# Kernel optimization log

Hardware: AMD Instinct MI355X
Metric: run time of the kernel (lower is better)

The kernel has to match this reference:

```python
import jax, jax.numpy as jnp
import numpy as np

B, N, D, H, CD = 2, 2048, 1024, 16, 3
HD = D // H


def setup_inputs() -> dict:
    key = jax.random.key(0)
    ks = jax.random.split(key, 6)
    x = jax.random.normal(ks[0], (B, N, D), dtype=jnp.float32)
    coords = jax.random.normal(ks[1], (B, N, CD), dtype=jnp.float32)
    attn_bias = jax.random.normal(ks[2], (N, N), dtype=jnp.float32) * 0.1
    Wqkv = jax.random.normal(ks[3], (D, 3 * D), dtype=jnp.float32) * (1.0 / np.sqrt(D))
    bqkv = jnp.zeros((3 * D,), dtype=jnp.float32)
    rel_weight = jax.random.normal(ks[4], (H, CD), dtype=jnp.float32) * 0.02
    return {"x": x, "coords": coords, "attn_bias": attn_bias, "Wqkv": Wqkv,
            "bqkv": bqkv, "rel_weight": rel_weight}


def reference(x, coords, attn_bias, Wqkv, bqkv, rel_weight):
    b, n, d = x.shape
    h, hd = H, HD
    qkv = x @ Wqkv + bqkv                       # (B,N,3D)
    q, k, v = jnp.split(qkv, 3, axis=-1)
    # reshape_for_mha: (B,N,D) -> (B,H,N,hd)
    def heads(t):
        return t.reshape(b, n, h, hd).transpose(0, 2, 1, 3)
    qh, kh, vh = heads(q), heads(k), heads(v)
    # coord_proj[b,h,n] = coords[b,n,:] @ rel_weight[h,:]
    coord_proj = jnp.einsum('bnc,hc->bhn', coords.astype(jnp.float32), rel_weight)
    # flex_attention: scale by 1/sqrt(head_dim) BEFORE score_mod
    scores = jnp.einsum('bhqd,bhkd->bhqk', qh, kh) / np.sqrt(hd)
    scores = scores + coord_proj[:, :, :, None] - coord_proj[:, :, None, :]
    scores = scores + attn_bias[None, None, :, :]   # '2d' additive mask bias
    attn = jax.nn.softmax(scores, axis=-1)
    yh = jnp.einsum('bhqk,bhkd->bhqd', attn, vh)    # (B,H,N,hd)
    return yh.transpose(0, 2, 1, 3).reshape(b, n, d)
```

## Files before the change

kernel.cpp:

```cpp
#include <hip/hip_runtime.h>
#include <hip/hip_bf16.h>
#include <math.h>

typedef __hip_bfloat16 bf16;
typedef __bf16  bf16x8 __attribute__((ext_vector_type(8)));
typedef float   f32x4  __attribute__((ext_vector_type(4)));

#define BB 2
#define NN 2048
#define DD 1024
#define HH 16
#define HD 64
#define LOG2E   1.44269504f
#define SCALE_Q 0.18033688f

__device__ __forceinline__ void glds16(const bf16* g, bf16* l) {
    __builtin_amdgcn_global_load_lds((const __attribute__((address_space(1))) void*)g,
                                     (__attribute__((address_space(3))) void*)l, 16, 0, 0);
}
__device__ __forceinline__ unsigned short bfu(float x) {
    bf16 b = __float2bfloat16(x);
    return __builtin_bit_cast(unsigned short, b);
}

__global__ __launch_bounds__(256) void prep(const float* __restrict__ x,
                                            const float* __restrict__ bias,
                                            const float* __restrict__ W,
                                            const float* __restrict__ coords,
                                            const float* __restrict__ relw,
                                            bf16* __restrict__ xb,
                                            float* __restrict__ pbf,
                                            bf16* __restrict__ Wt,
                                            bf16* __restrict__ cpn) {
    __shared__ bf16 tsm[64][65];
    const int bid = blockIdx.x, tid = threadIdx.x;
    if (bid < 2048) {
        size_t i = ((size_t)bid * 256 + tid) * 8;
        float4 a = *(const float4*)(x + i);
        float4 b = *(const float4*)(x + i + 4);
        bf16 t[8];
        t[0] = __float2bfloat16(a.x); t[1] = __float2bfloat16(a.y);
        t[2] = __float2bfloat16(a.z); t[3] = __float2bfloat16(a.w);
        t[4] = __float2bfloat16(b.x); t[5] = __float2bfloat16(b.y);
        t[6] = __float2bfloat16(b.z); t[7] = __float2bfloat16(b.w);
        *(int4*)(xb + i) = *(int4*)t;
    } else if (bid < 3072) {
        int t    = (bid - 2048) * 256 + tid;
        int lane = t & 63;
        int wave = (t >> 6) & 7;
        int kt   = (t >> 9) & 31;
        int Qb   = t >> 14;
        int quad = lane >> 4, l15 = lane & 15;
        float v[16];
#pragma unroll
        for (int j = 0; j < 16; ++j) {
            int g = j >> 2, r = j & 3;
            int q = Qb * 128 + wave * 16 + quad * 4 + r;
            int k = kt * 64 + g * 16 + l15;
            v[j] = LOG2E * bias[(size_t)q * NN + k];
        }
        int4* dst = (int4*)(pbf + (size_t)t * 16);
#pragma unroll
        for (int i = 0; i < 4; ++i) dst[i] = ((int4*)v)[i];
    } else if (bid < 3840) {
        int idx = bid - 3072;
        int n0 = (idx % 48) * 64;
        int k0 = (idx / 48) * 64;
        int tx = tid & 63, tg = tid >> 6;
#pragma unroll
        for (int i = 0; i < 16; ++i) {
            int r = tg + i * 4;
            tsm[r][tx] = __float2bfloat16(W[(size_t)(k0 + r) * 3072 + n0 + tx]);
        }
        __syncthreads();
#pragma unroll
        for (int i = 0; i < 16; ++i) {
            int r = tg + i * 4;
            Wt[(size_t)(n0 + r) * 1024 + k0 + tx] = tsm[tx][r];
        }
    } else {
        int idx = (bid - 3840) * 256 + tid;
        int n  = idx & (NN - 1);
        int bh = idx >> 11;
        int h  = bh & (HH - 1);
        int b  = bh >> 4;
        float acc = 0.f;
#pragma unroll
        for (int c = 0; c < 3; ++c)
            acc += coords[(size_t)(b * NN + n) * 3 + c] * relw[h * 3 + c];
        cpn[idx] = __float2bfloat16(-LOG2E * acc);
    }
}

__global__ __launch_bounds__(256) void qkv_gemm(const bf16* __restrict__ X,
                                                const bf16* __restrict__ W,
                                                const float* __restrict__ bq,
                                                bf16* __restrict__ qo,
                                                bf16* __restrict__ ko,
                                                bf16* __restrict__ vt) {
    __shared__ __align__(16) bf16 As[128 * 32];
    __shared__ __align__(16) bf16 Bs[128 * 32];
    const int tid  = threadIdx.x;
    const int n0   = blockIdx.x * 128;
    const int m0   = blockIdx.y * 128;
    const int wave = tid >> 6, lane = tid & 63, l15 = lane & 15, quad = lane >> 4;
    const int wm   = wave >> 1, wn = wave & 1;

    f32x4 acc[4][4];
    const f32x4 z4 = {0.f, 0.f, 0.f, 0.f};
#pragma unroll
    for (int i = 0; i < 4; ++i)
#pragma unroll
        for (int j = 0; j < 4; ++j) acc[i][j] = z4;

    for (int kt = 0; kt < 1024; kt += 32) {
        __syncthreads();
#pragma unroll
        for (int j = 0; j < 2; ++j) {
            int s   = (wave * 2 + j) * 64 + lane;
            int row = s >> 2;
            int c   = (s & 3) ^ ((row >> 1) & 3);
            glds16(X + (size_t)(m0 + row) * 1024 + kt + c * 8, As + (wave * 2 + j) * 512);
            glds16(W + (size_t)(n0 + row) * 1024 + kt + c * 8, Bs + (wave * 2 + j) * 512);
        }
        __syncthreads();

        bf16x8 a[4], b[4];
#pragma unroll
        for (int mt = 0; mt < 4; ++mt) {
            int ra = wm * 64 + mt * 16 + l15;
            a[mt] = *(const bf16x8*)&As[ra * 32 + ((quad ^ ((ra >> 1) & 3)) * 8)];
        }
#pragma unroll
        for (int nt = 0; nt < 4; ++nt) {
            int rb = wn * 64 + nt * 16 + l15;
            b[nt] = *(const bf16x8*)&Bs[rb * 32 + ((quad ^ ((rb >> 1) & 3)) * 8)];
        }
#pragma unroll
        for (int mt = 0; mt < 4; ++mt)
#pragma unroll
            for (int nt = 0; nt < 4; ++nt)
                acc[mt][nt] = __builtin_amdgcn_mfma_f32_16x16x32_bf16(a[mt], b[nt], acc[mt][nt], 0, 0, 0);
    }

#pragma unroll
    for (int nt = 0; nt < 4; ++nt) {
        int c    = n0 + wn * 64 + nt * 16 + l15;
        int tsel = c >> 10;
        int rem  = c & 1023;
        int h    = rem >> 6, d = rem & 63;
        float bias = bq[c];
        float qs   = (tsel == 0) ? SCALE_Q : 1.0f;
#pragma unroll
        for (int mt = 0; mt < 4; ++mt)
#pragma unroll
            for (int r = 0; r < 4; ++r) {
                int m = m0 + wm * 64 + mt * 16 + quad * 4 + r;
                int b = m >> 11, n = m & (NN - 1);
                bf16 val = __float2bfloat16((acc[mt][nt][r] + bias) * qs);
                if (tsel == 2)
                    vt[((size_t)(b * HH + h) * HD + d) * NN + n] = val;
                else
                    ((tsel == 1) ? ko : qo)[((size_t)(b * HH + h) * NN + n) * HD + d] = val;
            }
    }
}

__global__ __launch_bounds__(512, 4) void attn(const bf16* __restrict__ Q,
                                               const bf16* __restrict__ K,
                                               const bf16* __restrict__ Vt_g,
                                               const bf16* __restrict__ cpn_g,
                                               const float* __restrict__ pbf,
                                               float* __restrict__ out) {
    __shared__ __align__(16) bf16 Ks[2][64 * 64];
    __shared__ __align__(16) bf16 Vs[2][64 * 64];
    __shared__ __align__(16) unsigned PsW[8][16 * 36];
    __shared__ __align__(16) bf16 cpl[NN];
    const int tid  = threadIdx.x;
    const int Qb   = blockIdx.x;
    const int bh   = blockIdx.y;
    const int b    = bh >> 4, h = bh & 15;
    const int q0   = Qb * 128;
    const int wave = tid >> 6, lane = tid & 63, l15 = lane & 15, quad = lane >> 4;
    const size_t base = (size_t)bh * NN * HD;

    if (wave < 4)
        glds16(cpn_g + bh * NN + (wave * 64 + lane) * 8, cpl + wave * 512);

    const int qrow = q0 + wave * 16 + l15;
    bf16x8 qf0 = *(const bf16x8*)&Q[base + (size_t)qrow * HD + quad * 8];
    bf16x8 qf1 = *(const bf16x8*)&Q[base + (size_t)qrow * HD + 32 + quad * 8];

    const int ps   = wave * 64 + lane;
    const int prow = ps >> 3;
    const int pcol = (ps & 7) ^ (prow & 7);

    glds16(K    + base + (size_t)prow * HD + pcol * 8, Ks[0] + wave * 512);
    glds16(Vt_g + base + (size_t)prow * NN + pcol * 8, Vs[0] + wave * 512);

    const float* bptr = pbf + ((((size_t)Qb * 32) * 8 + wave) * 64 + lane) * 16;
    float4 bvA[4], bvB[4];
#pragma unroll
    for (int i = 0; i < 4; ++i) bvA[i] = ((const float4*)bptr)[i];

    const f32x4 z4 = {0.f, 0.f, 0.f, 0.f};
    f32x4 l4 = z4;
    f32x4 o[4];
#pragma unroll
    for (int t = 0; t < 4; ++t) o[t] = z4;

#define ATTN_TILE(T, CUR, BVC, BVN)                                               \
    {                                                                             \
        __syncthreads();     \
        if ((T) < 31) {                   \
            int kk1 = ((T) + 1) * 64;                                             \
            glds16(K    + base + (size_t)(kk1 + prow) * HD + pcol * 8,            \
                   Ks[(CUR) ^ 1] + wave * 512);                                   \
            glds16(Vt_g + base + (size_t)prow * NN + kk1 + pcol * 8,              \
                   Vs[(CUR) ^ 1] + wave * 512);                                   \
            const float* bp = bptr + (size_t)((T) + 1) * 8192;                    \
            BVN[0] = ((const float4*)bp)[0];                                      \
            BVN[1] = ((const float4*)bp)[1];                                      \
            BVN[2] = ((const float4*)bp)[2];                                      \
            BVN[3] = ((const float4*)bp)[3];                                      \
        }                                                                         \
            \
        f32x4 p4[4];                                                              \
        _Pragma("unroll")                                                         \
        for (int g = 0; g < 4; ++g) {                                             \
            float mgv = __bfloat162float(cpl[(T) * 64 + g * 16 + l15]);           \
            f32x4 mg4 = {mgv, mgv, mgv, mgv};                                     \
            f32x4 c0  = __builtin_bit_cast(f32x4, BVC[g]) + mg4;                  \
            int krow = g * 16 + l15, sw = krow & 7;                               \
            bf16x8 k0 = *(const bf16x8*)&Ks[(CUR)][krow * 64 + ((quad ^ sw) * 8)];         \
            bf16x8 k1 = *(const bf16x8*)&Ks[(CUR)][krow * 64 + (((4 + quad) ^ sw) * 8)];   \
            f32x4 s4 = __builtin_amdgcn_mfma_f32_16x16x32_bf16(qf0, k0, c0, 0, 0, 0);      \
            s4 = __builtin_amdgcn_mfma_f32_16x16x32_bf16(qf1, k1, s4, 0, 0, 0);   \
            f32x4 e;                                                              \
            e[0] = __builtin_amdgcn_exp2f(s4[0]);                                 \
            e[1] = __builtin_amdgcn_exp2f(s4[1]);                                 \
            e[2] = __builtin_amdgcn_exp2f(s4[2]);                                 \
            e[3] = __builtin_amdgcn_exp2f(s4[3]);                                 \
            p4[g] = e;                                                            \
            l4 = l4 + e;                                                          \
        }                                                                         \
                  \
        _Pragma("unroll")                                                         \
        for (int g2 = 0; g2 < 2; ++g2)                                            \
            _Pragma("unroll")                                                     \
            for (int r = 0; r < 4; ++r) {                                         \
                unsigned pk = (unsigned)bfu(p4[g2][r]) |                          \
                              ((unsigned)bfu(p4[g2 + 2][r]) << 16);               \
                PsW[wave][(quad * 4 + r) * 36 + g2 * 16 + l15] = pk;              \
            }                                                                     \
        asm volatile("s_waitcnt lgkmcnt(0)" ::: "memory");                        \
        const int4* pr = (const int4*)&PsW[wave][l15 * 36 + quad * 8];            \
        int4 da = pr[0], db = pr[1];                                              \
        union { unsigned u[4]; bf16x8 v; } u0, u1;                                \
        u0.u[0] = __builtin_amdgcn_perm(da.y, da.x, 0x05040100u);                 \
        u0.u[1] = __builtin_amdgcn_perm(da.w, da.z, 0x05040100u);                 \
        u0.u[2] = __builtin_amdgcn_perm(db.y, db.x, 0x05040100u);                 \
        u0.u[3] = __builtin_amdgcn_perm(db.w, db.z, 0x05040100u);                 \
        u1.u[0] = __builtin_amdgcn_perm(da.y, da.x, 0x07060302u);                 \
        u1.u[1] = __builtin_amdgcn_perm(da.w, da.z, 0x07060302u);                 \
        u1.u[2] = __builtin_amdgcn_perm(db.y, db.x, 0x07060302u);                 \
        u1.u[3] = __builtin_amdgcn_perm(db.w, db.z, 0x07060302u);                 \
                                              \
        __builtin_amdgcn_s_setprio(1);                                            \
        _Pragma("unroll")                                                         \
        for (int tt = 0; tt < 4; ++tt) {                                          \
            int drow = tt * 16 + l15, sw2 = drow & 7;                             \
            bf16x8 v0 = *(const bf16x8*)&Vs[(CUR)][drow * 64 + ((quad ^ sw2) * 8)];        \
            bf16x8 v1 = *(const bf16x8*)&Vs[(CUR)][drow * 64 + (((4 + quad) ^ sw2) * 8)];  \
            o[tt] = __builtin_amdgcn_mfma_f32_16x16x32_bf16(u0.v, v0, o[tt], 0, 0, 0);     \
            o[tt] = __builtin_amdgcn_mfma_f32_16x16x32_bf16(u1.v, v1, o[tt], 0, 0, 0);     \
        }                                                                         \
        __builtin_amdgcn_s_setprio(0);                                            \
    }

    for (int t = 0; t < 32; t += 2) {
        ATTN_TILE(t,     0, bvA, bvB)
        ATTN_TILE(t + 1, 1, bvB, bvA)
    }
#undef ATTN_TILE

    float l_loc[4] = {l4[0], l4[1], l4[2], l4[3]};
#pragma unroll
    for (int r = 0; r < 4; ++r) {
#pragma unroll
        for (int d = 1; d < 16; d <<= 1)
            l_loc[r] += __shfl_xor(l_loc[r], d, 64);
        float inv = 1.0f / l_loc[r];
        int qq = q0 + wave * 16 + quad * 4 + r;
#pragma unroll
        for (int tt = 0; tt < 4; ++tt)
            out[((size_t)(b * NN + qq)) * DD + h * HD + tt * 16 + l15] =
                o[tt][r] * inv;
    }
}

extern "C" void kernel_launch(void* const* d_in, const int* in_sizes, int n_in,
                              void* d_out, int out_size, void* d_ws, size_t ws_size,
                              hipStream_t stream) {
    const float* x      = (const float*)d_in[0];
    const float* coords = (const float*)d_in[1];
    const float* abias  = (const float*)d_in[2];
    const float* Wqkv   = (const float*)d_in[3];
    const float* bqkv   = (const float*)d_in[4];
    const float* relw   = (const float*)d_in[5];
    float* out = (float*)d_out;

    char* ws = (char*)d_ws;
    bf16*  xb  = (bf16*)(ws);
    bf16*  qw  = (bf16*)(ws + 8388608);
    bf16*  kw  = (bf16*)(ws + 16777216);
    bf16*  vt  = (bf16*)(ws + 25165824);
    bf16*  Wt  = (bf16*)(ws + 33554432);
    float* pbf = (float*)(ws + 39845888);
    bf16*  cpb = (bf16*)(ws + 56623104);

    prep    <<<dim3(4096),   256, 0, stream>>>(x, abias, Wqkv, coords, relw,
                                               xb, pbf, Wt, cpb);
    qkv_gemm<<<dim3(24, 32), 256, 0, stream>>>(xb, Wt, bqkv, qw, kw, vt);
    attn    <<<dim3(16, 32), 512, 0, stream>>>(qw, kw, vt, cpb, pbf, out);
}
```

Baseline: 203.5 us.

## Split attention key tiles across wave pairs with 64-query blocks and LDS reduction

Each attention block now covers 64 queries instead of 128, which doubles the grid. The two waves of a pair each handle half of every 64-key tile and merge their partial outputs and row sums through shared memory at the end. The bias prep kernel rewrites the pre-swizzled bias layout to match, and launch bounds are raised to allow more resident blocks. The aim is more parallelism and occupancy, at the cost of loading K/V once per 64 queries instead of once per 128, plus an extra reduction with two barriers.

```diff
diff --git a/kernel.cpp b/kernel.cpp
--- a/kernel.cpp
+++ b/kernel.cpp
@@ -45,21 +45,21 @@
         t[6] = __float2bfloat16(b.z); t[7] = __float2bfloat16(b.w);
         *(int4*)(xb + i) = *(int4*)t;
     } else if (bid < 3072) {
-        int t    = (bid - 2048) * 256 + tid;
-        int lane = t & 63;
-        int wave = (t >> 6) & 7;
-        int kt   = (t >> 9) & 31;
-        int Qb   = t >> 14;
-        int quad = lane >> 4, l15 = lane & 15;
+        int f0 = ((bid - 2048) * 256 + tid) * 16;
         float v[16];
 #pragma unroll
-        for (int j = 0; j < 16; ++j) {
-            int g = j >> 2, r = j & 3;
-            int q = Qb * 128 + wave * 16 + quad * 4 + r;
-            int k = kt * 64 + g * 16 + l15;
-            v[j] = LOG2E * bias[(size_t)q * NN + k];
-        }
-        int4* dst = (int4*)(pbf + (size_t)t * 16);
+        for (int u = 0; u < 16; ++u) {
+            int f    = f0 + u;
+            int j    = f & 7;
+            int lane = (f >> 3) & 63;
+            int wave = (f >> 9) & 7;
+            int t    = (f >> 12) & 31;
+            int Qb   = f >> 17;
+            int q = Qb * 64 + ((wave >> 1) << 4) + ((lane >> 4) << 2) + (j & 3);
+            int k = t * 64 + ((wave & 1) << 5) + ((j >> 2) << 4) + (lane & 15);
+            v[u] = LOG2E * bias[(size_t)q * NN + k];
+        }
+        int4* dst = (int4*)(pbf + (size_t)f0);
 #pragma unroll
         for (int i = 0; i < 4; ++i) dst[i] = ((int4*)v)[i];
     } else if (bid < 3840) {
@@ -166,7 +166,7 @@
     }
 }
 
-__global__ __launch_bounds__(512, 4) void attn(const bf16* __restrict__ Q,
+__global__ __launch_bounds__(512, 6) void attn(const bf16* __restrict__ Q,
                                                const bf16* __restrict__ K,
                                                const bf16* __restrict__ Vt_g,
                                                const bf16* __restrict__ cpn_g,
@@ -174,20 +174,21 @@
                                                float* __restrict__ out) {
     __shared__ __align__(16) bf16 Ks[2][64 * 64];
     __shared__ __align__(16) bf16 Vs[2][64 * 64];
-    __shared__ __align__(16) unsigned PsW[8][16 * 36];
+    __shared__ __align__(16) unsigned PsW[8][16 * 20];
     __shared__ __align__(16) bf16 cpl[NN];
     const int tid  = threadIdx.x;
     const int Qb   = blockIdx.x;
     const int bh   = blockIdx.y;
     const int b    = bh >> 4, h = bh & 15;
-    const int q0   = Qb * 128;
+    const int q0   = Qb * 64;
     const int wave = tid >> 6, lane = tid & 63, l15 = lane & 15, quad = lane >> 4;
+    const int wq   = wave >> 1, ws = wave & 1;
     const size_t base = (size_t)bh * NN * HD;
 
     if (wave < 4)
         glds16(cpn_g + bh * NN + (wave * 64 + lane) * 8, cpl + wave * 512);
 
-    const int qrow = q0 + wave * 16 + l15;
+    const int qrow = q0 + wq * 16 + l15;
     bf16x8 qf0 = *(const bf16x8*)&Q[base + (size_t)qrow * HD + quad * 8];
     bf16x8 qf1 = *(const bf16x8*)&Q[base + (size_t)qrow * HD + 32 + quad * 8];
 
@@ -198,10 +199,10 @@
     glds16(K    + base + (size_t)prow * HD + pcol * 8, Ks[0] + wave * 512);
     glds16(Vt_g + base + (size_t)prow * NN + pcol * 8, Vs[0] + wave * 512);
 
-    const float* bptr = pbf + ((((size_t)Qb * 32) * 8 + wave) * 64 + lane) * 16;
-    float4 bvA[4], bvB[4];
-#pragma unroll
-    for (int i = 0; i < 4; ++i) bvA[i] = ((const float4*)bptr)[i];
+    const float* bptr = pbf + (((size_t)(Qb * 32) * 8 + wave) * 64 + lane) * 8;
+    float4 bvA[2], bvB[2];
+    bvA[0] = ((const float4*)bptr)[0];
+    bvA[1] = ((const float4*)bptr)[1];
 
     const f32x4 z4 = {0.f, 0.f, 0.f, 0.f};
     f32x4 l4 = z4;
@@ -218,20 +219,18 @@
                    Ks[(CUR) ^ 1] + wave * 512);                                   \
             glds16(Vt_g + base + (size_t)prow * NN + kk1 + pcol * 8,              \
                    Vs[(CUR) ^ 1] + wave * 512);                                   \
-            const float* bp = bptr + (size_t)((T) + 1) * 8192;                    \
+            const float* bp = bptr + (size_t)((T) + 1) * 4096;                    \
             BVN[0] = ((const float4*)bp)[0];                                      \
             BVN[1] = ((const float4*)bp)[1];                                      \
-            BVN[2] = ((const float4*)bp)[2];                                      \
-            BVN[3] = ((const float4*)bp)[3];                                      \
         }                                                                         \
-            \
-        f32x4 p4[4];                                                              \
+                       \
+        f32x4 p4[2];                                                              \
         _Pragma("unroll")                                                         \
-        for (int g = 0; g < 4; ++g) {                                             \
-            float mgv = __bfloat162float(cpl[(T) * 64 + g * 16 + l15]);           \
+        for (int g = 0; g < 2; ++g) {                                             \
+            float mgv = __bfloat162float(cpl[(T) * 64 + ws * 32 + g * 16 + l15]); \
             f32x4 mg4 = {mgv, mgv, mgv, mgv};                                     \
             f32x4 c0  = __builtin_bit_cast(f32x4, BVC[g]) + mg4;                  \
-            int krow = g * 16 + l15, sw = krow & 7;                               \
+            int krow = ws * 32 + g * 16 + l15, sw = krow & 7;                     \
             bf16x8 k0 = *(const bf16x8*)&Ks[(CUR)][krow * 64 + ((quad ^ sw) * 8)];         \
             bf16x8 k1 = *(const bf16x8*)&Ks[(CUR)][krow * 64 + (((4 + quad) ^ sw) * 8)];   \
             f32x4 s4 = __builtin_amdgcn_mfma_f32_16x16x32_bf16(qf0, k0, c0, 0, 0, 0);      \
@@ -244,36 +243,28 @@
             p4[g] = e;                                                            \
             l4 = l4 + e;                                                          \
         }                                                                         \
-                  \
+           \
         _Pragma("unroll")                                                         \
-        for (int g2 = 0; g2 < 2; ++g2)                                            \
-            _Pragma("unroll")                                                     \
-            for (int r = 0; r < 4; ++r) {                                         \
-                unsigned pk = (unsigned)bfu(p4[g2][r]) |                          \
-                              ((unsigned)bfu(p4[g2 + 2][r]) << 16);               \
-                PsW[wave][(quad * 4 + r) * 36 + g2 * 16 + l15] = pk;              \
-            }                                                                     \
+        for (int r = 0; r < 4; ++r) {                                             \
+            unsigned pk = (unsigned)bfu(p4[0][r]) | ((unsigned)bfu(p4[1][r]) << 16); \
+            PsW[wave][(quad * 4 + r) * 20 + l15] = pk;                            \
+        }                                                                         \
         asm volatile("s_waitcnt lgkmcnt(0)" ::: "memory");                        \
-        const int4* pr = (const int4*)&PsW[wave][l15 * 36 + quad * 8];            \
+        const int4* pr = (const int4*)&PsW[wave][l15 * 20 + (quad & 1) * 8];      \
         int4 da = pr[0], db = pr[1];                                              \
-        union { unsigned u[4]; bf16x8 v; } u0, u1;                                \
-        u0.u[0] = __builtin_amdgcn_perm(da.y, da.x, 0x05040100u);                 \
-        u0.u[1] = __builtin_amdgcn_perm(da.w, da.z, 0x05040100u);                 \
-        u0.u[2] = __builtin_amdgcn_perm(db.y, db.x, 0x05040100u);                 \
-        u0.u[3] = __builtin_amdgcn_perm(db.w, db.z, 0x05040100u);                 \
-        u1.u[0] = __builtin_amdgcn_perm(da.y, da.x, 0x07060302u);                 \
-        u1.u[1] = __builtin_amdgcn_perm(da.w, da.z, 0x07060302u);                 \
-        u1.u[2] = __builtin_amdgcn_perm(db.y, db.x, 0x07060302u);                 \
-        u1.u[3] = __builtin_amdgcn_perm(db.w, db.z, 0x07060302u);                 \
-                                              \
+        union { unsigned u[4]; bf16x8 v; } uu;                                    \
+        unsigned sel = (quad < 2) ? 0x05040100u : 0x07060302u;                    \
+        uu.u[0] = __builtin_amdgcn_perm(da.y, da.x, sel);                         \
+        uu.u[1] = __builtin_amdgcn_perm(da.w, da.z, sel);                         \
+        uu.u[2] = __builtin_amdgcn_perm(db.y, db.x, sel);                         \
+        uu.u[3] = __builtin_amdgcn_perm(db.w, db.z, sel);                         \
+                                        \
         __builtin_amdgcn_s_setprio(1);                                            \
         _Pragma("unroll")                                                         \
         for (int tt = 0; tt < 4; ++tt) {                                          \
             int drow = tt * 16 + l15, sw2 = drow & 7;                             \
-            bf16x8 v0 = *(const bf16x8*)&Vs[(CUR)][drow * 64 + ((quad ^ sw2) * 8)];        \
-            bf16x8 v1 = *(const bf16x8*)&Vs[(CUR)][drow * 64 + (((4 + quad) ^ sw2) * 8)];  \
-            o[tt] = __builtin_amdgcn_mfma_f32_16x16x32_bf16(u0.v, v0, o[tt], 0, 0, 0);     \
-            o[tt] = __builtin_amdgcn_mfma_f32_16x16x32_bf16(u1.v, v1, o[tt], 0, 0, 0);     \
+            bf16x8 vf = *(const bf16x8*)&Vs[(CUR)][drow * 64 + (((ws * 4 + quad) ^ sw2) * 8)]; \
+            o[tt] = __builtin_amdgcn_mfma_f32_16x16x32_bf16(uu.v, vf, o[tt], 0, 0, 0);     \
         }                                                                         \
         __builtin_amdgcn_s_setprio(0);                                            \
     }
@@ -286,16 +277,38 @@
 
     float l_loc[4] = {l4[0], l4[1], l4[2], l4[3]};
 #pragma unroll
-    for (int r = 0; r < 4; ++r) {
+    for (int r = 0; r < 4; ++r)
 #pragma unroll
         for (int d = 1; d < 16; d <<= 1)
             l_loc[r] += __shfl_xor(l_loc[r], d, 64);
-        float inv = 1.0f / l_loc[r];
-        int qq = q0 + wave * 16 + quad * 4 + r;
-#pragma unroll
-        for (int tt = 0; tt < 4; ++tt)
-            out[((size_t)(b * NN + qq)) * DD + h * HD + tt * 16 + l15] =
-                o[tt][r] * inv;
+
+    float* obase = (wq < 2) ? (float*)Ks : (float*)Vs;
+    const int rowl0 = (wq & 1) * 16;
+    __syncthreads();
+    if (ws == 1) {
+#pragma unroll
+        for (int r = 0; r < 4; ++r) {
+            int row = rowl0 + quad * 4 + r;
+#pragma unroll
+            for (int tt = 0; tt < 4; ++tt)
+                obase[row * 68 + tt * 16 + l15] = o[tt][r];
+            if (l15 == 0) obase[row * 68 + 64] = l_loc[r];
+        }
+    }
+    __syncthreads();
+    if (ws == 0) {
+#pragma unroll
+        for (int r = 0; r < 4; ++r) {
+            int row = rowl0 + quad * 4 + r;
+            float lt  = l_loc[r] + obase[row * 68 + 64];
+            float inv = 1.0f / lt;
+            int qq = q0 + wq * 16 + quad * 4 + r;
+#pragma unroll
+            for (int tt = 0; tt < 4; ++tt) {
+                float ov = o[tt][r] + obase[row * 68 + tt * 16 + l15];
+                out[((size_t)(b * NN + qq)) * DD + h * HD + tt * 16 + l15] = ov * inv;
+            }
+        }
     }
 }
 
@@ -322,5 +335,5 @@
     prep    <<<dim3(4096),   256, 0, stream>>>(x, abias, Wqkv, coords, relw,
                                                xb, pbf, Wt, cpb);
     qkv_gemm<<<dim3(24, 32), 256, 0, stream>>>(xb, Wt, bqkv, qw, kw, vt);
-    attn    <<<dim3(16, 32), 512, 0, stream>>>(qw, kw, vt, cpb, pbf, out);
-}
+    attn    <<<dim3(32, 32), 512, 0, stream>>>(qw, kw, vt, cpb, pbf, out);
+}
```

Result: slower. 232.8 us (+14.4%).

## Process two 16-row query tiles per wave in attention, halve block size

Applied to the files above, without the earlier changes.

Each wave now handles 32 query rows (two 16-row sub-tiles) instead of 16. The K and V fragments read from LDS are reused across both sub-tiles, and the block shrinks from 512 to 256 threads. The bias pre-layout in the prep kernel is reordered to match the new per-wave fragment mapping. This cuts LDS read traffic and synchronisation per unit of work, at the cost of more registers per thread and fewer waves per block to hide latency.

```diff
diff --git a/kernel.cpp b/kernel.cpp
--- a/kernel.cpp
+++ b/kernel.cpp
@@ -45,21 +45,22 @@
         t[6] = __float2bfloat16(b.z); t[7] = __float2bfloat16(b.w);
         *(int4*)(xb + i) = *(int4*)t;
     } else if (bid < 3072) {
-        int t    = (bid - 2048) * 256 + tid;
-        int lane = t & 63;
-        int wave = (t >> 6) & 7;
-        int kt   = (t >> 9) & 31;
-        int Qb   = t >> 14;
-        int quad = lane >> 4, l15 = lane & 15;
+        int f0 = ((bid - 2048) * 256 + tid) * 16;
         float v[16];
 #pragma unroll
-        for (int j = 0; j < 16; ++j) {
-            int g = j >> 2, r = j & 3;
-            int q = Qb * 128 + wave * 16 + quad * 4 + r;
-            int k = kt * 64 + g * 16 + l15;
-            v[j] = LOG2E * bias[(size_t)q * NN + k];
-        }
-        int4* dst = (int4*)(pbf + (size_t)t * 16);
+        for (int u = 0; u < 16; ++u) {
+            int f    = f0 + u;
+            int j    = f & 15;
+            int lane = (f >> 4) & 63;
+            int qh   = (f >> 10) & 1;
+            int w    = (f >> 11) & 3;
+            int t    = (f >> 13) & 31;
+            int Qb   = f >> 18;
+            int q = Qb * 128 + w * 32 + qh * 16 + ((lane >> 4) << 2) + (j & 3);
+            int k = t * 64 + ((j >> 2) << 4) + (lane & 15);
+            v[u] = LOG2E * bias[(size_t)q * NN + k];
+        }
+        int4* dst = (int4*)(pbf + (size_t)f0);
 #pragma unroll
         for (int i = 0; i < 4; ++i) dst[i] = ((int4*)v)[i];
     } else if (bid < 3840) {
@@ -166,7 +167,7 @@
     }
 }
 
-__global__ __launch_bounds__(512, 4) void attn(const bf16* __restrict__ Q,
+__global__ __launch_bounds__(256, 2) void attn(const bf16* __restrict__ Q,
                                                const bf16* __restrict__ K,
                                                const bf16* __restrict__ Vt_g,
                                                const bf16* __restrict__ cpn_g,
@@ -174,128 +175,195 @@
                                                float* __restrict__ out) {
     __shared__ __align__(16) bf16 Ks[2][64 * 64];
     __shared__ __align__(16) bf16 Vs[2][64 * 64];
-    __shared__ __align__(16) unsigned PsW[8][16 * 36];
+    __shared__ __align__(16) unsigned PsW[4][16 * 36];
     __shared__ __align__(16) bf16 cpl[NN];
     const int tid  = threadIdx.x;
     const int Qb   = blockIdx.x;
     const int bh   = blockIdx.y;
     const int b    = bh >> 4, h = bh & 15;
     const int q0   = Qb * 128;
-    const int wave = tid >> 6, lane = tid & 63, l15 = lane & 15, quad = lane >> 4;
+    const int w    = tid >> 6, lane = tid & 63, l15 = lane & 15, quad = lane >> 4;
     const size_t base = (size_t)bh * NN * HD;
 
-    if (wave < 4)
-        glds16(cpn_g + bh * NN + (wave * 64 + lane) * 8, cpl + wave * 512);
-
-    const int qrow = q0 + wave * 16 + l15;
-    bf16x8 qf0 = *(const bf16x8*)&Q[base + (size_t)qrow * HD + quad * 8];
-    bf16x8 qf1 = *(const bf16x8*)&Q[base + (size_t)qrow * HD + 32 + quad * 8];
-
-    const int ps   = wave * 64 + lane;
-    const int prow = ps >> 3;
-    const int pcol = (ps & 7) ^ (prow & 7);
-
-    glds16(K    + base + (size_t)prow * HD + pcol * 8, Ks[0] + wave * 512);
-    glds16(Vt_g + base + (size_t)prow * NN + pcol * 8, Vs[0] + wave * 512);
-
-    const float* bptr = pbf + ((((size_t)Qb * 32) * 8 + wave) * 64 + lane) * 16;
-    float4 bvA[4], bvB[4];
-#pragma unroll
-    for (int i = 0; i < 4; ++i) bvA[i] = ((const float4*)bptr)[i];
+    glds16(cpn_g + bh * NN + (w * 64 + lane) * 8, cpl + w * 512);
+
+    const int qr0 = q0 + w * 32 + l15;
+    bf16x8 qf00 = *(const bf16x8*)&Q[base + (size_t)qr0 * HD + quad * 8];
+    bf16x8 qf01 = *(const bf16x8*)&Q[base + (size_t)qr0 * HD + 32 + quad * 8];
+    bf16x8 qf10 = *(const bf16x8*)&Q[base + (size_t)(qr0 + 16) * HD + quad * 8];
+    bf16x8 qf11 = *(const bf16x8*)&Q[base + (size_t)(qr0 + 16) * HD + 32 + quad * 8];
+
+#pragma unroll
+    for (int j = 0; j < 2; ++j) {
+        int s   = j * 256 + w * 64 + lane;
+        int row = s >> 3;
+        int c   = (s & 7) ^ (row & 7);
+        glds16(K    + base + (size_t)row * HD + c * 8, Ks[0] + j * 2048 + w * 512);
+        glds16(Vt_g + base + (size_t)row * NN + c * 8, Vs[0] + j * 2048 + w * 512);
+    }
+
+    const float* bptr = pbf + ((((size_t)Qb * 32 * 4 + w) * 2) * 64 + lane) * 16;
+    float4 bvA0[4], bvA1[4], bvB0[4], bvB1[4];
+#pragma unroll
+    for (int i = 0; i < 4; ++i) {
+        bvA0[i] = ((const float4*)bptr)[i];
+        bvA1[i] = ((const float4*)(bptr + 1024))[i];
+    }
 
     const f32x4 z4 = {0.f, 0.f, 0.f, 0.f};
-    f32x4 l4 = z4;
-    f32x4 o[4];
-#pragma unroll
-    for (int t = 0; t < 4; ++t) o[t] = z4;
-
-#define ATTN_TILE(T, CUR, BVC, BVN)                                               \
+    f32x4 l40 = z4, l41 = z4;
+    f32x4 o0[4], o1[4];
+#pragma unroll
+    for (int t = 0; t < 4; ++t) { o0[t] = z4; o1[t] = z4; }
+
+#define ATTN_TILE(T, CUR, BC0, BC1, BN0, BN1)                                     \
     {                                                                             \
         __syncthreads();     \
         if ((T) < 31) {                   \
             int kk1 = ((T) + 1) * 64;                                             \
-            glds16(K    + base + (size_t)(kk1 + prow) * HD + pcol * 8,            \
-                   Ks[(CUR) ^ 1] + wave * 512);                                   \
-            glds16(Vt_g + base + (size_t)prow * NN + kk1 + pcol * 8,              \
-                   Vs[(CUR) ^ 1] + wave * 512);                                   \
+            _Pragma("unroll")                                                     \
+            for (int j = 0; j < 2; ++j) {                                         \
+                int s   = j * 256 + w * 64 + lane;                                \
+                int row = s >> 3;                                                 \
+                int c   = (s & 7) ^ (row & 7);                                    \
+                glds16(K    + base + (size_t)(kk1 + row) * HD + c * 8,            \
+                       Ks[(CUR) ^ 1] + j * 2048 + w * 512);                       \
+                glds16(Vt_g + base + (size_t)row * NN + kk1 + c * 8,              \
+                       Vs[(CUR) ^ 1] + j * 2048 + w * 512);                       \
+            }                                                                     \
             const float* bp = bptr + (size_t)((T) + 1) * 8192;                    \
-            BVN[0] = ((const float4*)bp)[0];                                      \
-            BVN[1] = ((const float4*)bp)[1];                                      \
-            BVN[2] = ((const float4*)bp)[2];                                      \
-            BVN[3] = ((const float4*)bp)[3];                                      \
-        }                                                                         \
-            \
-        f32x4 p4[4];                                                              \
+            BN0[0] = ((const float4*)bp)[0];                                      \
+            BN0[1] = ((const float4*)bp)[1];                                      \
+            BN0[2] = ((const float4*)bp)[2];                                      \
+            BN0[3] = ((const float4*)bp)[3];                                      \
+            BN1[0] = ((const float4*)(bp + 1024))[0];                             \
+            BN1[1] = ((const float4*)(bp + 1024))[1];                             \
+            BN1[2] = ((const float4*)(bp + 1024))[2];                             \
+            BN1[3] = ((const float4*)(bp + 1024))[3];                             \
+        }                                                                         \
+                \
+        f32x4 p0[4], p1[4];                                                       \
         _Pragma("unroll")                                                         \
         for (int g = 0; g < 4; ++g) {                                             \
             float mgv = __bfloat162float(cpl[(T) * 64 + g * 16 + l15]);           \
             f32x4 mg4 = {mgv, mgv, mgv, mgv};                                     \
-            f32x4 c0  = __builtin_bit_cast(f32x4, BVC[g]) + mg4;                  \
+            f32x4 c00 = __builtin_bit_cast(f32x4, BC0[g]) + mg4;                  \
+            f32x4 c01 = __builtin_bit_cast(f32x4, BC1[g]) + mg4;                  \
             int krow = g * 16 + l15, sw = krow & 7;                               \
             bf16x8 k0 = *(const bf16x8*)&Ks[(CUR)][krow * 64 + ((quad ^ sw) * 8)];         \
             bf16x8 k1 = *(const bf16x8*)&Ks[(CUR)][krow * 64 + (((4 + quad) ^ sw) * 8)];   \
-            f32x4 s4 = __builtin_amdgcn_mfma_f32_16x16x32_bf16(qf0, k0, c0, 0, 0, 0);      \
-            s4 = __builtin_amdgcn_mfma_f32_16x16x32_bf16(qf1, k1, s4, 0, 0, 0);   \
-            f32x4 e;                                                              \
-            e[0] = __builtin_amdgcn_exp2f(s4[0]);                                 \
-            e[1] = __builtin_amdgcn_exp2f(s4[1]);                                 \
-            e[2] = __builtin_amdgcn_exp2f(s4[2]);                                 \
-            e[3] = __builtin_amdgcn_exp2f(s4[3]);                                 \
-            p4[g] = e;                                                            \
-            l4 = l4 + e;                                                          \
-        }                                                                         \
-                  \
+            f32x4 s0 = __builtin_amdgcn_mfma_f32_16x16x32_bf16(qf00, k0, c00, 0, 0, 0);    \
+            s0 = __builtin_amdgcn_mfma_f32_16x16x32_bf16(qf01, k1, s0, 0, 0, 0);  \
+            f32x4 s1 = __builtin_amdgcn_mfma_f32_16x16x32_bf16(qf10, k0, c01, 0, 0, 0);    \
+            s1 = __builtin_amdgcn_mfma_f32_16x16x32_bf16(qf11, k1, s1, 0, 0, 0);  \
+            f32x4 e0, e1;                                                         \
+            e0[0] = __builtin_amdgcn_exp2f(s0[0]);                                \
+            e0[1] = __builtin_amdgcn_exp2f(s0[1]);                                \
+            e0[2] = __builtin_amdgcn_exp2f(s0[2]);                                \
+            e0[3] = __builtin_amdgcn_exp2f(s0[3]);                                \
+            e1[0] = __builtin_amdgcn_exp2f(s1[0]);                                \
+            e1[1] = __builtin_amdgcn_exp2f(s1[1]);                                \
+            e1[2] = __builtin_amdgcn_exp2f(s1[2]);                                \
+            e1[3] = __builtin_amdgcn_exp2f(s1[3]);                                \
+            p0[g] = e0; l40 = l40 + e0;                                           \
+            p1[g] = e1; l41 = l41 + e1;                                           \
+        }                                                                         \
+                         \
         _Pragma("unroll")                                                         \
         for (int g2 = 0; g2 < 2; ++g2)                                            \
             _Pragma("unroll")                                                     \
             for (int r = 0; r < 4; ++r) {                                         \
-                unsigned pk = (unsigned)bfu(p4[g2][r]) |                          \
-                              ((unsigned)bfu(p4[g2 + 2][r]) << 16);               \
-                PsW[wave][(quad * 4 + r) * 36 + g2 * 16 + l15] = pk;              \
+                unsigned pk = (unsigned)bfu(p0[g2][r]) |                          \
+                              ((unsigned)bfu(p0[g2 + 2][r]) << 16);               \
+                PsW[w][(quad * 4 + r) * 36 + g2 * 16 + l15] = pk;                 \
             }                                                                     \
         asm volatile("s_waitcnt lgkmcnt(0)" ::: "memory");                        \
-        const int4* pr = (const int4*)&PsW[wave][l15 * 36 + quad * 8];            \
-        int4 da = pr[0], db = pr[1];                                              \
-        union { unsigned u[4]; bf16x8 v; } u0, u1;                                \
-        u0.u[0] = __builtin_amdgcn_perm(da.y, da.x, 0x05040100u);                 \
-        u0.u[1] = __builtin_amdgcn_perm(da.w, da.z, 0x05040100u);                 \
-        u0.u[2] = __builtin_amdgcn_perm(db.y, db.x, 0x05040100u);                 \
-        u0.u[3] = __builtin_amdgcn_perm(db.w, db.z, 0x05040100u);                 \
-        u1.u[0] = __builtin_amdgcn_perm(da.y, da.x, 0x07060302u);                 \
-        u1.u[1] = __builtin_amdgcn_perm(da.w, da.z, 0x07060302u);                 \
-        u1.u[2] = __builtin_amdgcn_perm(db.y, db.x, 0x07060302u);                 \
-        u1.u[3] = __builtin_amdgcn_perm(db.w, db.z, 0x07060302u);                 \
-                                              \
-        __builtin_amdgcn_s_setprio(1);                                            \
+        union { unsigned u[4]; bf16x8 v; } uA0, uA1;                              \
+        {                                                                         \
+            const int4* pr = (const int4*)&PsW[w][l15 * 36 + quad * 8];           \
+            int4 da = pr[0], db = pr[1];                                          \
+            uA0.u[0] = __builtin_amdgcn_perm(da.y, da.x, 0x05040100u);            \
+            uA0.u[1] = __builtin_amdgcn_perm(da.w, da.z, 0x05040100u);            \
+            uA0.u[2] = __builtin_amdgcn_perm(db.y, db.x, 0x05040100u);            \
+            uA0.u[3] = __builtin_amdgcn_perm(db.w, db.z, 0x05040100u);            \
+            uA1.u[0] = __builtin_amdgcn_perm(da.y, da.x, 0x07060302u);            \
+            uA1.u[1] = __builtin_amdgcn_perm(da.w, da.z, 0x07060302u);            \
+            uA1.u[2] = __builtin_amdgcn_perm(db.y, db.x, 0x07060302u);            \
+            uA1.u[3] = __builtin_amdgcn_perm(db.w, db.z, 0x07060302u);            \
+        }                                                                         \
+                         \
+        bf16x8 vf0[4], vf1[4];                                                    \
         _Pragma("unroll")                                                         \
         for (int tt = 0; tt < 4; ++tt) {                                          \
             int drow = tt * 16 + l15, sw2 = drow & 7;                             \
-            bf16x8 v0 = *(const bf16x8*)&Vs[(CUR)][drow * 64 + ((quad ^ sw2) * 8)];        \
-            bf16x8 v1 = *(const bf16x8*)&Vs[(CUR)][drow * 64 + (((4 + quad) ^ sw2) * 8)];  \
-            o[tt] = __builtin_amdgcn_mfma_f32_16x16x32_bf16(u0.v, v0, o[tt], 0, 0, 0);     \
-            o[tt] = __builtin_amdgcn_mfma_f32_16x16x32_bf16(u1.v, v1, o[tt], 0, 0, 0);     \
+            vf0[tt] = *(const bf16x8*)&Vs[(CUR)][drow * 64 + ((quad ^ sw2) * 8)];          \
+            vf1[tt] = *(const bf16x8*)&Vs[(CUR)][drow * 64 + (((4 + quad) ^ sw2) * 8)];    \
+        }                                                                         \
+                                                                  \
+        __builtin_amdgcn_s_setprio(1);                                            \
+        _Pragma("unroll")                                                         \
+        for (int tt = 0; tt < 4; ++tt) {                                          \
+            o0[tt] = __builtin_amdgcn_mfma_f32_16x16x32_bf16(uA0.v, vf0[tt], o0[tt], 0, 0, 0); \
+            o0[tt] = __builtin_amdgcn_mfma_f32_16x16x32_bf16(uA1.v, vf1[tt], o0[tt], 0, 0, 0); \
         }                                                                         \
         __builtin_amdgcn_s_setprio(0);                                            \
+                     \
+        _Pragma("unroll")                                                         \
+        for (int g2 = 0; g2 < 2; ++g2)                                            \
+            _Pragma("unroll")                                                     \
+            for (int r = 0; r < 4; ++r) {                                         \
+                unsigned pk = (unsigned)bfu(p1[g2][r]) |                          \
+                              ((unsigned)bfu(p1[g2 + 2][r]) << 16);               \
+                PsW[w][(quad * 4 + r) * 36 + g2 * 16 + l15] = pk;                 \
+            }                                                                     \
+        asm volatile("s_waitcnt lgkmcnt(0)" ::: "memory");                        \
+        union { unsigned u[4]; bf16x8 v; } uB0, uB1;                              \
+        {                                                                         \
+            const int4* pr = (const int4*)&PsW[w][l15 * 36 + quad * 8];           \
+            int4 da = pr[0], db = pr[1];                                          \
+            uB0.u[0] = __builtin_amdgcn_perm(da.y, da.x, 0x05040100u);            \
+            uB0.u[1] = __builtin_amdgcn_perm(da.w, da.z, 0x05040100u);            \
+            uB0.u[2] = __builtin_amdgcn_perm(db.y, db.x, 0x05040100u);            \
+            uB0.u[3] = __builtin_amdgcn_perm(db.w, db.z, 0x05040100u);            \
+            uB1.u[0] = __builtin_amdgcn_perm(da.y, da.x, 0x07060302u);            \
+            uB1.u[1] = __builtin_amdgcn_perm(da.w, da.z, 0x07060302u);            \
+            uB1.u[2] = __builtin_amdgcn_perm(db.y, db.x, 0x07060302u);            \
+            uB1.u[3] = __builtin_amdgcn_perm(db.w, db.z, 0x07060302u);            \
+        }                                                                         \
+                                                 \
+        __builtin_amdgcn_s_setprio(1);                                            \
+        _Pragma("unroll")                                                         \
+        for (int tt = 0; tt < 4; ++tt) {                                          \
+            o1[tt] = __builtin_amdgcn_mfma_f32_16x16x32_bf16(uB0.v, vf0[tt], o1[tt], 0, 0, 0); \
+            o1[tt] = __builtin_amdgcn_mfma_f32_16x16x32_bf16(uB1.v, vf1[tt], o1[tt], 0, 0, 0); \
+        }                                                                         \
+        __builtin_amdgcn_s_setprio(0);                                            \
     }
 
     for (int t = 0; t < 32; t += 2) {
-        ATTN_TILE(t,     0, bvA, bvB)
-        ATTN_TILE(t + 1, 1, bvB, bvA)
+        ATTN_TILE(t,     0, bvA0, bvA1, bvB0, bvB1)
+        ATTN_TILE(t + 1, 1, bvB0, bvB1, bvA0, bvA1)
     }
 #undef ATTN_TILE
 
-    float l_loc[4] = {l4[0], l4[1], l4[2], l4[3]};
+    float la[4] = {l40[0], l40[1], l40[2], l40[3]};
+    float lb[4] = {l41[0], l41[1], l41[2], l41[3]};
 #pragma unroll
     for (int r = 0; r < 4; ++r) {
 #pragma unroll
-        for (int d = 1; d < 16; d <<= 1)
-            l_loc[r] += __shfl_xor(l_loc[r], d, 64);
-        float inv = 1.0f / l_loc[r];
-        int qq = q0 + wave * 16 + quad * 4 + r;
-#pragma unroll
-        for (int tt = 0; tt < 4; ++tt)
-            out[((size_t)(b * NN + qq)) * DD + h * HD + tt * 16 + l15] =
-                o[tt][r] * inv;
+        for (int d = 1; d < 16; d <<= 1) {
+            la[r] += __shfl_xor(la[r], d, 64);
+            lb[r] += __shfl_xor(lb[r], d, 64);
+        }
+        float inva = 1.0f / la[r];
+        float invb = 1.0f / lb[r];
+        int qa = q0 + w * 32 + quad * 4 + r;
+        int qb2 = qa + 16;
+#pragma unroll
+        for (int tt = 0; tt < 4; ++tt) {
+            out[((size_t)(b * NN + qa))  * DD + h * HD + tt * 16 + l15] = o0[tt][r] * inva;
+            out[((size_t)(b * NN + qb2)) * DD + h * HD + tt * 16 + l15] = o1[tt][r] * invb;
+        }
     }
 }
 
@@ -322,5 +390,5 @@
     prep    <<<dim3(4096),   256, 0, stream>>>(x, abias, Wqkv, coords, relw,
                                                xb, pbf, Wt, cpb);
     qkv_gemm<<<dim3(24, 32), 256, 0, stream>>>(xb, Wt, bqkv, qw, kw, vt);
-    attn    <<<dim3(16, 32), 512, 0, stream>>>(qw, kw, vt, cpb, pbf, out);
-}
+    attn    <<<dim3(16, 32), 256, 0, stream>>>(qw, kw, vt, cpb, pbf, out);
+}
```

Measured after the change: 205.7 us. Within noise of the previous version (+1.1%).
